# Performance work log

Hardware: AMD Instinct MI355X
Metric: run time of the kernel (lower is better)

The kernel has to match this reference:

```python
import jax, jax.numpy as jnp
import numpy as np

B, T, C = 2, 2048, 1024
NUM_HEADS = 16
HEAD_DIM = C // NUM_HEADS
TEMP = 1.0
LN_EPS = 1e-6


def setup_inputs() -> dict:
    key = jax.random.key(0)
    kx, kqw, kpw = jax.random.split(key, 3)
    x = jax.random.normal(kx, (B, T, C), dtype=jnp.float32)
    # causal mask, broadcastable to [B, H, T, T]
    mask = jnp.tril(jnp.ones((T, T), dtype=bool))[None, None, :, :]
    # LayerNorm params (flax defaults: scale=1, bias=0)
    ln_scale = jnp.ones((C,), dtype=jnp.float32)
    ln_bias = jnp.zeros((C,), dtype=jnp.float32)
    # xavier_uniform init for dense kernels, zero bias (torch_linear)
    lim_qkv = float(np.sqrt(6.0 / (C + 3 * C)))
    qkv_w = jax.random.uniform(kqw, (C, 3 * C), jnp.float32, -lim_qkv, lim_qkv)
    qkv_b = jnp.zeros((3 * C,), dtype=jnp.float32)
    lim_p = float(np.sqrt(6.0 / (C + C)))
    proj_w = jax.random.uniform(kpw, (C, C), jnp.float32, -lim_p, lim_p)
    proj_b = jnp.zeros((C,), dtype=jnp.float32)
    return {"x": x, "mask": mask, "ln_scale": ln_scale, "ln_bias": ln_bias,
            "qkv_w": qkv_w, "qkv_b": qkv_b, "proj_w": proj_w, "proj_b": proj_b}


def reference(x, mask, ln_scale, ln_bias, qkv_w, qkv_b, proj_w, proj_b):
    b, t, c = x.shape
    # LayerNorm (eps=1e-6, flax default)
    mu = jnp.mean(x, axis=-1, keepdims=True)
    var = jnp.mean(jnp.square(x - mu), axis=-1, keepdims=True)
    xn = (x - mu) * jax.lax.rsqrt(var + LN_EPS) * ln_scale + ln_bias
    # fused QKV projection
    qkv = xn @ qkv_w + qkv_b
    q, k, v = jnp.split(qkv, 3, axis=-1)
    q = q.reshape(b, t, NUM_HEADS, HEAD_DIM) / TEMP
    k = k.reshape(b, t, NUM_HEADS, HEAD_DIM)
    v = v.reshape(b, t, NUM_HEADS, HEAD_DIM)
    # scaled dot-product attention with mask (eval path: no dropout)
    q = q / jnp.sqrt(jnp.float32(HEAD_DIM)).astype(x.dtype)
    scores = jnp.einsum('bqhd,bkhd->bhqk', q, k)  # [B,H,T,T]
    big_neg = jnp.finfo(x.dtype).min
    scores = jnp.where(mask, scores, big_neg)
    attn_weights = jax.nn.softmax(scores, axis=-1).astype(x.dtype)
    out = jnp.einsum('bhqk,bkhd->bqhd', attn_weights, v).reshape(b, t, c)
    return out @ proj_w + proj_b
```

## Files before the change

kernel.cpp:

```cpp
#include <hip/hip_runtime.h>
#include <cstdint>
#include <math.h>

#define DEV __device__ __forceinline__

typedef unsigned int u32;
typedef unsigned short u16;
typedef __attribute__((ext_vector_type(4))) float f32x4;
typedef __attribute__((ext_vector_type(4))) u32 u32x4;
typedef __attribute__((ext_vector_type(2))) u32 u32x2;
typedef __attribute__((ext_vector_type(8))) __bf16 bf16x8;

static_assert(sizeof(bf16x8) == 16, "bf16x8 must be 16B");

static constexpr int Tn = 2048, Cn = 1024;
static constexpr int Mrows = 2 * Tn;
static constexpr float QSCALE2 = 0.125f * 1.44269504088896f;

DEV u16 f2bf_rne(float f) {
  u32 u = __builtin_bit_cast(u32, f);
  u32 r = u + 0x7fffu + ((u >> 16) & 1u);
  return (u16)(r >> 16);
}
DEV float bf2f(u16 h) {
  u32 u = ((u32)h) << 16;
  return __builtin_bit_cast(float, u);
}
DEV u32 pack2bf(float a, float b) {
  return (u32)f2bf_rne(a) | ((u32)f2bf_rne(b) << 16);
}
DEV float fexp2(float x) {
#if __has_builtin(__builtin_amdgcn_exp2f)
  return __builtin_amdgcn_exp2f(x);
#else
  return exp2f(x);
#endif
}

DEV void stage16(const void* g, void* l) {
#if __has_builtin(__builtin_amdgcn_global_load_lds)
  __builtin_amdgcn_global_load_lds(
      (__attribute__((address_space(1))) u32*)(uintptr_t)g,
      (__attribute__((address_space(3))) u32*)l, 16, 0, 0);
#else
  *(u32x4*)l = *(const u32x4*)g;
#endif
}

__global__ __launch_bounds__(256) void ln_kernel(const float* __restrict__ x,
                                                 const float* __restrict__ sc,
                                                 const float* __restrict__ bi,
                                                 u16* __restrict__ xn) {
  int row = blockIdx.x;
  int t = threadIdx.x;
  const float* xr = x + (size_t)row * Cn;
  f32x4 v = *(const f32x4*)(xr + t * 4);
  float s = v.x + v.y + v.z + v.w;
  float s2 = v.x * v.x + v.y * v.y + v.z * v.z + v.w * v.w;
#pragma unroll
  for (int off = 1; off < 64; off <<= 1) {
    s += __shfl_xor(s, off);
    s2 += __shfl_xor(s2, off);
  }
  __shared__ float red[8];
  if ((t & 63) == 0) {
    red[(t >> 6) * 2] = s;
    red[(t >> 6) * 2 + 1] = s2;
  }
  __syncthreads();
  s = red[0] + red[2] + red[4] + red[6];
  s2 = red[1] + red[3] + red[5] + red[7];
  float mean = s * (1.0f / Cn);
  float var = s2 * (1.0f / Cn) - mean * mean;
  float rstd = rsqrtf(var + 1e-6f);
  f32x4 g = *(const f32x4*)(sc + t * 4);
  f32x4 b = *(const f32x4*)(bi + t * 4);
  u32 lo = pack2bf((v.x - mean) * rstd * g.x + b.x, (v.y - mean) * rstd * g.y + b.y);
  u32 hi = pack2bf((v.z - mean) * rstd * g.z + b.z, (v.w - mean) * rstd * g.w + b.w);
  u32x2 pack = {lo, hi};
  *(u32x2*)(xn + (size_t)row * Cn + t * 4) = pack;
}

__global__ __launch_bounds__(256) void transpose_cast2(const float* __restrict__ qkv_w,
                                                       u16* __restrict__ wqkv,
                                                       const float* __restrict__ proj_w,
                                                       u16* __restrict__ wproj) {
  __shared__ float tile[32][33];
  int bx = blockIdx.x;
  const float* src;
  u16* dst;
  int Cc;
  if (bx < 96) {
    src = qkv_w; dst = wqkv; Cc = 3072;
  } else {
    src = proj_w; dst = wproj; Cc = 1024; bx -= 96;
  }
  int tx = threadIdx.x, ty = threadIdx.y;
  int c0 = bx * 32, r0 = blockIdx.y * 32;
#pragma unroll
  for (int k = 0; k < 4; ++k)
    tile[ty + 8 * k][tx] = src[(size_t)(r0 + ty + 8 * k) * Cc + c0 + tx];
  __syncthreads();
#pragma unroll
  for (int k = 0; k < 4; ++k)
    dst[(size_t)(c0 + ty + 8 * k) * 1024 + r0 + tx] = f2bf_rne(tile[tx][ty + 8 * k]);
}

__global__ __launch_bounds__(256) void vt_prep(const u16* __restrict__ qkvm,
                                               u16* __restrict__ vt) {
  __shared__ u16 tile[32][33];
  int bh = blockIdx.z;
  int b = bh >> 4, h = bh & 15;
  int t0 = blockIdx.x * 32, d0 = blockIdx.y * 32;
  int tx = threadIdx.x, ty = threadIdx.y;
#pragma unroll
  for (int k = 0; k < 4; ++k)
    tile[ty + 8 * k][tx] =
        qkvm[(size_t)(b * Tn + t0 + ty + 8 * k) * 3072 + 2 * Cn + h * 64 + d0 + tx];
  __syncthreads();
#pragma unroll
  for (int k = 0; k < 4; ++k)
    vt[((size_t)bh * 64 + d0 + ty + 8 * k) * 2048 + t0 + tx] = tile[tx][ty + 8 * k];
}

template <bool OUT_F32, bool QKV_SCALE>
__global__ __launch_bounds__(256, 3) void gemm_kernel(const u16* __restrict__ A,
                                                      const u16* __restrict__ Bt,
                                                      const float* __restrict__ bias,
                                                      void* __restrict__ Cout,
                                                      int Nsz, int Ksz) {
  __shared__ u16 As[128 * 32];
  __shared__ u16 Bs[128 * 32];
  int t = threadIdx.x;
  int l = t & 63, w = t >> 6;
  int quad = l >> 4, c16 = l & 15;
  int wm = w & 1, wn = w >> 1;
  int m0 = blockIdx.y * 128, n0 = blockIdx.x * 128;

  f32x4 acc[4][4];
#pragma unroll
  for (int mt = 0; mt < 4; ++mt)
#pragma unroll
    for (int nt = 0; nt < 4; ++nt) acc[mt][nt] = (f32x4){0.f, 0.f, 0.f, 0.f};

  for (int kk = 0; kk < Ksz; kk += 32) {
#pragma unroll
    for (int i = 0; i < 2; ++i) {
      int c = t + i * 256;
      int m = c >> 2, k8 = (c & 3) ^ ((m >> 1) & 3);
      stage16(A + (size_t)(m0 + m) * Ksz + kk + k8 * 8, (char*)As + c * 16);
    }
#pragma unroll
    for (int i = 0; i < 2; ++i) {
      int c = t + i * 256;
      int n = c >> 2, k8 = (c & 3) ^ ((n >> 1) & 3);
      stage16(Bt + (size_t)(n0 + n) * Ksz + kk + k8 * 8, (char*)Bs + c * 16);
    }
    __syncthreads();
    bf16x8 af[4], bf[4];
#pragma unroll
    for (int mt = 0; mt < 4; ++mt) {
      int m = wm * 64 + mt * 16 + c16;
      int LC = m * 4 + (quad ^ ((m >> 1) & 3));
      af[mt] = *(const bf16x8*)((const char*)As + LC * 16);
    }
#pragma unroll
    for (int nt = 0; nt < 4; ++nt) {
      int n = wn * 64 + nt * 16 + c16;
      int LC = n * 4 + (quad ^ ((n >> 1) & 3));
      bf[nt] = *(const bf16x8*)((const char*)Bs + LC * 16);
    }
#pragma unroll
    for (int mt = 0; mt < 4; ++mt)
#pragma unroll
      for (int nt = 0; nt < 4; ++nt)
        acc[mt][nt] = __builtin_amdgcn_mfma_f32_16x16x32_bf16(af[mt], bf[nt],
                                                              acc[mt][nt], 0, 0, 0);
    __syncthreads();
  }
#pragma unroll
  for (int mt = 0; mt < 4; ++mt) {
    int row = m0 + wm * 64 + mt * 16 + quad * 4;
#pragma unroll
    for (int nt = 0; nt < 4; ++nt) {
      int col = n0 + wn * 64 + nt * 16 + c16;
      float bv = bias[col];
      float scale = (QKV_SCALE && col < 1024) ? QSCALE2 : 1.0f;
#pragma unroll
      for (int r = 0; r < 4; ++r) {
        float v = (acc[mt][nt][r] + bv) * scale;
        if (OUT_F32)
          ((float*)Cout)[(size_t)(row + r) * Nsz + col] = v;
        else
          ((u16*)Cout)[(size_t)(row + r) * Nsz + col] = f2bf_rne(v);
      }
    }
  }
}

__constant__ int4 chunk_tab[24] = {
    {15, 0, 8, 0}, {15, 8, 8, 1}, {14, 0, 8, 0}, {7, 0, 8, -1},
    {14, 8, 7, 1}, {13, 0, 7, 0}, {13, 7, 7, 1}, {12, 0, 7, 0}, {6, 0, 7, -1},
    {12, 7, 6, 1}, {11, 0, 6, 0}, {11, 6, 6, 1}, {10, 0, 6, 0}, {5, 0, 6, -1},
    {10, 6, 5, 1}, {9, 0, 5, 0}, {9, 5, 5, 1}, {8, 0, 5, 0}, {4, 0, 5, -1},
    {8, 5, 4, 1}, {3, 0, 4, -1},
    {2, 0, 3, -1},
    {1, 0, 2, -1},
    {0, 0, 1, -1}};

__global__ __launch_bounds__(256, 2) void flash_kernel(const u16* __restrict__ qkv,
                                                       const u16* __restrict__ vt,
                                                       u16* __restrict__ aout,
                                                       u16* __restrict__ Op,
                                                       float* __restrict__ ml) {
  int4 ck = chunk_tab[blockIdx.x >> 5];
  int bh = blockIdx.x & 31;
  int qt = ck.x, k0 = ck.y, kend = ck.y + ck.z, half = ck.w;
  int b = bh >> 4, h = bh & 15;
  int t = threadIdx.x, l = t & 63, w = t >> 6;
  int quad = l >> 4, c16 = l & 15;
  int q0 = qt * 128;
  const u16* __restrict__ vtb = vt + (size_t)bh * 64 * 2048;

  __shared__ u16 Ks[128 * 64];
  __shared__ u16 Ps[128 * 128];

  bf16x8 qf[2][2];
#pragma unroll
  for (int nt = 0; nt < 2; ++nt)
#pragma unroll
    for (int ks = 0; ks < 2; ++ks)
      qf[nt][ks] = *(const bf16x8*)(qkv +
          (size_t)(b * Tn + q0 + w * 32 + nt * 16 + c16) * 3072 +
          h * 64 + ks * 32 + quad * 8);

  float mrow[2] = {-1e30f, -1e30f};
  float lrow[2] = {0.f, 0.f};
  f32x4 o[2][4];
#pragma unroll
  for (int mq = 0; mq < 2; ++mq)
#pragma unroll
    for (int dt = 0; dt < 4; ++dt) o[mq][dt] = (f32x4){0.f, 0.f, 0.f, 0.f};

  for (int kt = k0; kt < kend; ++kt) {
#pragma unroll
    for (int i = 0; i < 4; ++i) {
      int c = t + i * 256;
      int key = c >> 3, d8 = (c & 7) ^ (key & 7);
      stage16(qkv + (size_t)(b * Tn + kt * 128 + key) * 3072 + Cn + h * 64 + d8 * 8,
              (char*)Ks + c * 16);
    }
    bf16x8 vfc[4], vfn[4];
#pragma unroll
    for (int dt = 0; dt < 4; ++dt)
      vfc[dt] = *(const bf16x8*)(vtb + (size_t)(dt * 16 + c16) * 2048 + kt * 128 +
                                 quad * 8);
    __syncthreads();

    f32x4 s[8][2];
#pragma unroll
    for (int mt = 0; mt < 8; ++mt)
#pragma unroll
      for (int nt = 0; nt < 2; ++nt) s[mt][nt] = (f32x4){0.f, 0.f, 0.f, 0.f};
#pragma unroll
    for (int mt = 0; mt < 8; ++mt) {
#pragma unroll
      for (int ks = 0; ks < 2; ++ks) {
        int key = mt * 16 + c16;
        int d8 = ks * 4 + quad;
        int LC = key * 8 + (d8 ^ (key & 7));
        bf16x8 kf = *(const bf16x8*)((const char*)Ks + LC * 16);
#pragma unroll
        for (int nt = 0; nt < 2; ++nt)
          s[mt][nt] = __builtin_amdgcn_mfma_f32_16x16x32_bf16(kf, qf[nt][ks],
                                                              s[mt][nt], 0, 0, 0);
      }
    }
    if (kt == qt) {
#pragma unroll
      for (int mt = 0; mt < 8; ++mt)
#pragma unroll
        for (int nt = 0; nt < 2; ++nt)
#pragma unroll
          for (int r = 0; r < 4; ++r) {
            int key = kt * 128 + mt * 16 + quad * 4 + r;
            int q = q0 + w * 32 + nt * 16 + c16;
            if (key > q) s[mt][nt][r] = -1e30f;
          }
    }
    float alph[2];
#pragma unroll
    for (int nt = 0; nt < 2; ++nt) {
      float rm = -1e30f;
#pragma unroll
      for (int mt = 0; mt < 8; ++mt)
#pragma unroll
        for (int r = 0; r < 4; ++r) rm = fmaxf(rm, s[mt][nt][r]);
      rm = fmaxf(rm, __shfl_xor(rm, 16));
      rm = fmaxf(rm, __shfl_xor(rm, 32));
      float mnew = fmaxf(mrow[nt], rm);
      alph[nt] = fexp2(mrow[nt] - mnew);
      mrow[nt] = mnew;
      float rs = 0.f;
#pragma unroll
      for (int mt = 0; mt < 8; ++mt)
#pragma unroll
        for (int r = 0; r < 4; ++r) {
          float e = fexp2(s[mt][nt][r] - mnew);
          s[mt][nt][r] = e;
          rs += e;
        }
      rs += __shfl_xor(rs, 16);
      rs += __shfl_xor(rs, 32);
      lrow[nt] = lrow[nt] * alph[nt] + rs;
    }
#pragma unroll
    for (int mq = 0; mq < 2; ++mq)
#pragma unroll
      for (int r = 0; r < 4; ++r) {
        float a = __shfl(alph[mq], quad * 4 + r);
#pragma unroll
        for (int dt = 0; dt < 4; ++dt) o[mq][dt][r] *= a;
      }
#pragma unroll
    for (int mt = 0; mt < 8; ++mt)
#pragma unroll
      for (int nt = 0; nt < 2; ++nt) {
        int q = w * 32 + nt * 16 + c16;
        int kc = mt * 4 + quad;
        int LC = q * 32 + (kc ^ ((q & 15) << 1));
        u32x2 pk = {pack2bf(s[mt][nt][0], s[mt][nt][1]),
                    pack2bf(s[mt][nt][2], s[mt][nt][3])};
        *(u32x2*)((char*)Ps + LC * 8) = pk;
      }
#pragma unroll
    for (int ks = 0; ks < 4; ++ks) {
      if (ks < 3) {
#pragma unroll
        for (int dt = 0; dt < 4; ++dt)
          vfn[dt] = *(const bf16x8*)(vtb + (size_t)(dt * 16 + c16) * 2048 +
                                     kt * 128 + (ks + 1) * 32 + quad * 8);
      }
      bf16x8 pa[2];
#pragma unroll
      for (int mq = 0; mq < 2; ++mq) {
        int q = w * 32 + mq * 16 + c16;
        int kc = ks * 8 + quad * 2;
        int LC = q * 32 + (kc ^ ((q & 15) << 1));
        pa[mq] = *(const bf16x8*)((const char*)Ps + LC * 8);
      }
#pragma unroll
      for (int dt = 0; dt < 4; ++dt)
#pragma unroll
        for (int mq = 0; mq < 2; ++mq)
          o[mq][dt] = __builtin_amdgcn_mfma_f32_16x16x32_bf16(pa[mq], vfc[dt],
                                                              o[mq][dt], 0, 0, 0);
#pragma unroll
      for (int dt = 0; dt < 4; ++dt) vfc[dt] = vfn[dt];
    }
    __syncthreads();
  }

  float linv[2] = {1.0f / lrow[0], 1.0f / lrow[1]};
  if (half < 0) {
#pragma unroll
    for (int mq = 0; mq < 2; ++mq)
#pragma unroll
      for (int r = 0; r < 4; ++r) {
        float li = __shfl(linv[mq], quad * 4 + r);
        int q = q0 + w * 32 + mq * 16 + quad * 4 + r;
#pragma unroll
        for (int dt = 0; dt < 4; ++dt)
          aout[(size_t)(b * Tn + q) * 1024 + h * 64 + dt * 16 + c16] =
              f2bf_rne(o[mq][dt][r] * li);
      }
  } else {
    int ps = ((qt - 8) * 32 + bh) * 2 + half;
#pragma unroll
    for (int mq = 0; mq < 2; ++mq)
#pragma unroll
      for (int r = 0; r < 4; ++r) {
        float li = __shfl(linv[mq], quad * 4 + r);
        int qr = w * 32 + mq * 16 + quad * 4 + r;
#pragma unroll
        for (int dt = 0; dt < 4; ++dt)
          Op[((size_t)ps * 128 + qr) * 64 + dt * 16 + c16] =
              f2bf_rne(o[mq][dt][r] * li);
      }
    if (quad == 0) {
#pragma unroll
      for (int nt = 0; nt < 2; ++nt) {
        int qr = w * 32 + nt * 16 + c16;
        ml[((size_t)ps * 128 + qr) * 2] = mrow[nt];
        ml[((size_t)ps * 128 + qr) * 2 + 1] = lrow[nt];
      }
    }
  }
}

__global__ __launch_bounds__(256) void combine_kernel(const u16* __restrict__ Op,
                                                      const float* __restrict__ ml,
                                                      u16* __restrict__ aout) {
  int qt = 8 + (blockIdx.x >> 5);
  int bh = blockIdx.x & 31;
  int b = bh >> 4, h = bh & 15;
  int ps0 = ((qt - 8) * 32 + bh) * 2;
  int d = threadIdx.x & 63, rq = threadIdx.x >> 6;
  for (int r = 0; r < 32; ++r) {
    int row = rq * 32 + r;
    float m0 = ml[((size_t)ps0 * 128 + row) * 2];
    float l0 = ml[((size_t)ps0 * 128 + row) * 2 + 1];
    float m1 = ml[((size_t)(ps0 + 1) * 128 + row) * 2];
    float l1 = ml[((size_t)(ps0 + 1) * 128 + row) * 2 + 1];
    float M = fmaxf(m0, m1);
    float w0 = fexp2(m0 - M) * l0, w1 = fexp2(m1 - M) * l1;
    float inv = 1.0f / (w0 + w1);
    float o0 = bf2f(Op[((size_t)ps0 * 128 + row) * 64 + d]);
    float o1 = bf2f(Op[((size_t)(ps0 + 1) * 128 + row) * 64 + d]);
    aout[(size_t)(b * Tn + qt * 128 + row) * 1024 + h * 64 + d] =
        f2bf_rne((w0 * o0 + w1 * o1) * inv);
  }
}

extern "C" void kernel_launch(void* const* d_in, const int* in_sizes, int n_in,
                              void* d_out, int out_size, void* d_ws, size_t ws_size,
                              hipStream_t stream) {
  const float* x = (const float*)d_in[0];
  const float* ln_s = (const float*)d_in[2];
  const float* ln_b = (const float*)d_in[3];
  const float* qkv_w = (const float*)d_in[4];
  const float* qkv_b = (const float*)d_in[5];
  const float* proj_w = (const float*)d_in[6];
  const float* proj_b = (const float*)d_in[7];
  float* out = (float*)d_out;
  char* ws = (char*)d_ws;

  u16* xn = (u16*)ws;
  u16* wqkv = (u16*)(ws + (8ull << 20));
  u16* wproj = (u16*)(ws + (14ull << 20));
  u16* qkvm = (u16*)(ws + (16ull << 20));
  u16* attn = (u16*)(ws + (40ull << 20));
  u16* vt = (u16*)(ws + (48ull << 20));
  u16* Op = (u16*)ws;
  float* ml = (float*)(ws + (8ull << 20));

  ln_kernel<<<Mrows, 256, 0, stream>>>(x, ln_s, ln_b, xn);
  transpose_cast2<<<dim3(128, 32), dim3(32, 8), 0, stream>>>(qkv_w, wqkv, proj_w,
                                                             wproj);
  gemm_kernel<false, true><<<dim3(24, 32), 256, 0, stream>>>(xn, wqkv, qkv_b, qkvm,
                                                             3072, 1024);
  vt_prep<<<dim3(64, 2, 32), dim3(32, 8), 0, stream>>>(qkvm, vt);
  flash_kernel<<<768, 256, 0, stream>>>(qkvm, vt, attn, Op, ml);
  combine_kernel<<<256, 256, 0, stream>>>(Op, ml, attn);
  gemm_kernel<true, false><<<dim3(8, 32), 256, 0, stream>>>(attn, wproj, proj_b, out,
                                                            1024, 1024);
}
```

Before: 234.6 us.

## Merge prep kernels, fuse V-transpose into QKV GEMM, load K directly from global

Combines the LayerNorm and weight transpose-cast kernels into one launch, and removes the separate vt_prep kernel by having the QKV GEMM epilogue write V already transposed. In the flash kernel, K tiles are no longer staged in LDS. Each wave loads K fragments straight from global memory with a double-buffered register prefetch, which drops the per-iteration LDS staging and one barrier. This trades fewer launches and less LDS traffic for redundant, less coalesced global K reads across waves and strided 8-byte V stores in the GEMM epilogue.

```diff
diff --git a/kernel.cpp b/kernel.cpp
--- a/kernel.cpp
+++ b/kernel.cpp
@@ -14,7 +14,6 @@
 static_assert(sizeof(bf16x8) == 16, "bf16x8 must be 16B");
 
 static constexpr int Tn = 2048, Cn = 1024;
-static constexpr int Mrows = 2 * Tn;
 static constexpr float QSCALE2 = 0.125f * 1.44269504088896f;
 
 DEV u16 f2bf_rne(float f) {
@@ -47,87 +46,73 @@
 #endif
 }
 
-__global__ __launch_bounds__(256) void ln_kernel(const float* __restrict__ x,
-                                                 const float* __restrict__ sc,
-                                                 const float* __restrict__ bi,
-                                                 u16* __restrict__ xn) {
-  int row = blockIdx.x;
+__global__ __launch_bounds__(256) void pre_kernel(const float* __restrict__ x,
+                                                  const float* __restrict__ sc,
+                                                  const float* __restrict__ bi,
+                                                  u16* __restrict__ xn,
+                                                  const float* __restrict__ qkv_w,
+                                                  u16* __restrict__ wqkv,
+                                                  const float* __restrict__ proj_w,
+                                                  u16* __restrict__ wproj) {
+  __shared__ float shm[32 * 33];
   int t = threadIdx.x;
-  const float* xr = x + (size_t)row * Cn;
-  f32x4 v = *(const f32x4*)(xr + t * 4);
-  float s = v.x + v.y + v.z + v.w;
-  float s2 = v.x * v.x + v.y * v.y + v.z * v.z + v.w * v.w;
-#pragma unroll
-  for (int off = 1; off < 64; off <<= 1) {
-    s += __shfl_xor(s, off);
-    s2 += __shfl_xor(s2, off);
-  }
-  __shared__ float red[8];
-  if ((t & 63) == 0) {
-    red[(t >> 6) * 2] = s;
-    red[(t >> 6) * 2 + 1] = s2;
-  }
-  __syncthreads();
-  s = red[0] + red[2] + red[4] + red[6];
-  s2 = red[1] + red[3] + red[5] + red[7];
-  float mean = s * (1.0f / Cn);
-  float var = s2 * (1.0f / Cn) - mean * mean;
-  float rstd = rsqrtf(var + 1e-6f);
-  f32x4 g = *(const f32x4*)(sc + t * 4);
-  f32x4 b = *(const f32x4*)(bi + t * 4);
-  u32 lo = pack2bf((v.x - mean) * rstd * g.x + b.x, (v.y - mean) * rstd * g.y + b.y);
-  u32 hi = pack2bf((v.z - mean) * rstd * g.z + b.z, (v.w - mean) * rstd * g.w + b.w);
-  u32x2 pack = {lo, hi};
-  *(u32x2*)(xn + (size_t)row * Cn + t * 4) = pack;
-}
-
-__global__ __launch_bounds__(256) void transpose_cast2(const float* __restrict__ qkv_w,
-                                                       u16* __restrict__ wqkv,
-                                                       const float* __restrict__ proj_w,
-                                                       u16* __restrict__ wproj) {
-  __shared__ float tile[32][33];
-  int bx = blockIdx.x;
-  const float* src;
-  u16* dst;
-  int Cc;
-  if (bx < 96) {
-    src = qkv_w; dst = wqkv; Cc = 3072;
+  if (blockIdx.x < 4096) {
+    int row = blockIdx.x;
+    const float* xr = x + (size_t)row * Cn;
+    f32x4 v = *(const f32x4*)(xr + t * 4);
+    float s = v.x + v.y + v.z + v.w;
+    float s2 = v.x * v.x + v.y * v.y + v.z * v.z + v.w * v.w;
+#pragma unroll
+    for (int off = 1; off < 64; off <<= 1) {
+      s += __shfl_xor(s, off);
+      s2 += __shfl_xor(s2, off);
+    }
+    if ((t & 63) == 0) {
+      shm[(t >> 6) * 2] = s;
+      shm[(t >> 6) * 2 + 1] = s2;
+    }
+    __syncthreads();
+    s = shm[0] + shm[2] + shm[4] + shm[6];
+    s2 = shm[1] + shm[3] + shm[5] + shm[7];
+    float mean = s * (1.0f / Cn);
+    float var = s2 * (1.0f / Cn) - mean * mean;
+    float rstd = rsqrtf(var + 1e-6f);
+    f32x4 g = *(const f32x4*)(sc + t * 4);
+    f32x4 b = *(const f32x4*)(bi + t * 4);
+    u32 lo = pack2bf((v.x - mean) * rstd * g.x + b.x, (v.y - mean) * rstd * g.y + b.y);
+    u32 hi = pack2bf((v.z - mean) * rstd * g.z + b.z, (v.w - mean) * rstd * g.w + b.w);
+    u32x2 pack = {lo, hi};
+    *(u32x2*)(xn + (size_t)row * Cn + t * 4) = pack;
   } else {
-    src = proj_w; dst = wproj; Cc = 1024; bx -= 96;
-  }
-  int tx = threadIdx.x, ty = threadIdx.y;
-  int c0 = bx * 32, r0 = blockIdx.y * 32;
-#pragma unroll
-  for (int k = 0; k < 4; ++k)
-    tile[ty + 8 * k][tx] = src[(size_t)(r0 + ty + 8 * k) * Cc + c0 + tx];
-  __syncthreads();
-#pragma unroll
-  for (int k = 0; k < 4; ++k)
-    dst[(size_t)(c0 + ty + 8 * k) * 1024 + r0 + tx] = f2bf_rne(tile[tx][ty + 8 * k]);
-}
-
-__global__ __launch_bounds__(256) void vt_prep(const u16* __restrict__ qkvm,
-                                               u16* __restrict__ vt) {
-  __shared__ u16 tile[32][33];
-  int bh = blockIdx.z;
-  int b = bh >> 4, h = bh & 15;
-  int t0 = blockIdx.x * 32, d0 = blockIdx.y * 32;
-  int tx = threadIdx.x, ty = threadIdx.y;
-#pragma unroll
-  for (int k = 0; k < 4; ++k)
-    tile[ty + 8 * k][tx] =
-        qkvm[(size_t)(b * Tn + t0 + ty + 8 * k) * 3072 + 2 * Cn + h * 64 + d0 + tx];
-  __syncthreads();
-#pragma unroll
-  for (int k = 0; k < 4; ++k)
-    vt[((size_t)bh * 64 + d0 + ty + 8 * k) * 2048 + t0 + tx] = tile[tx][ty + 8 * k];
-}
-
-template <bool OUT_F32, bool QKV_SCALE>
+    int idx = blockIdx.x - 4096;
+    int bx = idx & 127, by = idx >> 7;
+    const float* src;
+    u16* dst;
+    int Cc;
+    if (bx < 96) {
+      src = qkv_w; dst = wqkv; Cc = 3072;
+    } else {
+      src = proj_w; dst = wproj; Cc = 1024; bx -= 96;
+    }
+    int tx = t & 31, ty = t >> 5;
+    int c0 = bx * 32, r0 = by * 32;
+#pragma unroll
+    for (int k = 0; k < 4; ++k)
+      shm[(ty + 8 * k) * 33 + tx] = src[(size_t)(r0 + ty + 8 * k) * Cc + c0 + tx];
+    __syncthreads();
+#pragma unroll
+    for (int k = 0; k < 4; ++k)
+      dst[(size_t)(c0 + ty + 8 * k) * 1024 + r0 + tx] =
+          f2bf_rne(shm[tx * 33 + ty + 8 * k]);
+  }
+}
+
+template <bool OUT_F32, bool QKV>
 __global__ __launch_bounds__(256, 3) void gemm_kernel(const u16* __restrict__ A,
                                                       const u16* __restrict__ Bt,
                                                       const float* __restrict__ bias,
                                                       void* __restrict__ Cout,
+                                                      u16* __restrict__ vtp,
                                                       int Nsz, int Ksz) {
   __shared__ u16 As[128 * 32];
   __shared__ u16 Bs[128 * 32];
@@ -185,14 +170,22 @@
     for (int nt = 0; nt < 4; ++nt) {
       int col = n0 + wn * 64 + nt * 16 + c16;
       float bv = bias[col];
-      float scale = (QKV_SCALE && col < 1024) ? QSCALE2 : 1.0f;
-#pragma unroll
-      for (int r = 0; r < 4; ++r) {
-        float v = (acc[mt][nt][r] + bv) * scale;
-        if (OUT_F32)
-          ((float*)Cout)[(size_t)(row + r) * Nsz + col] = v;
-        else
-          ((u16*)Cout)[(size_t)(row + r) * Nsz + col] = f2bf_rne(v);
+      if (QKV && col >= 2048) {
+        int hd = col - 2048;
+        int bb = row >> 11, tt = row & 2047;
+        u32x2 pk = {pack2bf(acc[mt][nt][0] + bv, acc[mt][nt][1] + bv),
+                    pack2bf(acc[mt][nt][2] + bv, acc[mt][nt][3] + bv)};
+        *(u32x2*)(vtp + ((size_t)bb * 1024 + hd) * 2048 + tt) = pk;
+      } else {
+        float scale = (QKV && col < 1024) ? QSCALE2 : 1.0f;
+#pragma unroll
+        for (int r = 0; r < 4; ++r) {
+          float v = (acc[mt][nt][r] + bv) * scale;
+          if (OUT_F32)
+            ((float*)Cout)[(size_t)(row + r) * Nsz + col] = v;
+          else
+            ((u16*)Cout)[(size_t)(row + r) * Nsz + col] = f2bf_rne(v);
+        }
       }
     }
   }
@@ -221,8 +214,9 @@
   int quad = l >> 4, c16 = l & 15;
   int q0 = qt * 128;
   const u16* __restrict__ vtb = vt + (size_t)bh * 64 * 2048;
-
-  __shared__ u16 Ks[128 * 64];
+  const u16* __restrict__ kb =
+      qkv + ((size_t)(b * Tn) + c16) * 3072 + Cn + h * 64 + quad * 8;
+
   __shared__ u16 Ps[128 * 128];
 
   bf16x8 qf[2][2];
@@ -243,19 +237,18 @@
     for (int dt = 0; dt < 4; ++dt) o[mq][dt] = (f32x4){0.f, 0.f, 0.f, 0.f};
 
   for (int kt = k0; kt < kend; ++kt) {
-#pragma unroll
-    for (int i = 0; i < 4; ++i) {
-      int c = t + i * 256;
-      int key = c >> 3, d8 = (c & 7) ^ (key & 7);
-      stage16(qkv + (size_t)(b * Tn + kt * 128 + key) * 3072 + Cn + h * 64 + d8 * 8,
-              (char*)Ks + c * 16);
-    }
-    bf16x8 vfc[4], vfn[4];
+    bf16x8 vfc[4];
 #pragma unroll
     for (int dt = 0; dt < 4; ++dt)
       vfc[dt] = *(const bf16x8*)(vtb + (size_t)(dt * 16 + c16) * 2048 + kt * 128 +
                                  quad * 8);
-    __syncthreads();
+    const u16* kr = kb + (size_t)kt * 128 * 3072;
+    bf16x8 ka[2][2];
+#pragma unroll
+    for (int p = 0; p < 2; ++p)
+#pragma unroll
+      for (int ks = 0; ks < 2; ++ks)
+        ka[p][ks] = *(const bf16x8*)(kr + (size_t)p * 16 * 3072 + ks * 32);
 
     f32x4 s[8][2];
 #pragma unroll
@@ -265,15 +258,16 @@
 #pragma unroll
     for (int mt = 0; mt < 8; ++mt) {
 #pragma unroll
-      for (int ks = 0; ks < 2; ++ks) {
-        int key = mt * 16 + c16;
-        int d8 = ks * 4 + quad;
-        int LC = key * 8 + (d8 ^ (key & 7));
-        bf16x8 kf = *(const bf16x8*)((const char*)Ks + LC * 16);
+      for (int ks = 0; ks < 2; ++ks)
 #pragma unroll
         for (int nt = 0; nt < 2; ++nt)
-          s[mt][nt] = __builtin_amdgcn_mfma_f32_16x16x32_bf16(kf, qf[nt][ks],
-                                                              s[mt][nt], 0, 0, 0);
+          s[mt][nt] = __builtin_amdgcn_mfma_f32_16x16x32_bf16(
+              ka[mt & 1][ks], qf[nt][ks], s[mt][nt], 0, 0, 0);
+      if (mt < 6) {
+#pragma unroll
+        for (int ks = 0; ks < 2; ++ks)
+          ka[mt & 1][ks] =
+              *(const bf16x8*)(kr + (size_t)(mt + 2) * 16 * 3072 + ks * 32);
       }
     }
     if (kt == qt) {
@@ -335,6 +329,7 @@
       }
 #pragma unroll
     for (int ks = 0; ks < 4; ++ks) {
+      bf16x8 vfn[4];
       if (ks < 3) {
 #pragma unroll
         for (int dt = 0; dt < 4; ++dt)
@@ -355,10 +350,11 @@
         for (int mq = 0; mq < 2; ++mq)
           o[mq][dt] = __builtin_amdgcn_mfma_f32_16x16x32_bf16(pa[mq], vfc[dt],
                                                               o[mq][dt], 0, 0, 0);
-#pragma unroll
-      for (int dt = 0; dt < 4; ++dt) vfc[dt] = vfn[dt];
-    }
-    __syncthreads();
+      if (ks < 3) {
+#pragma unroll
+        for (int dt = 0; dt < 4; ++dt) vfc[dt] = vfn[dt];
+      }
+    }
   }
 
   float linv[2] = {1.0f / lrow[0], 1.0f / lrow[1]};
@@ -444,14 +440,12 @@
   u16* Op = (u16*)ws;
   float* ml = (float*)(ws + (8ull << 20));
 
-  ln_kernel<<<Mrows, 256, 0, stream>>>(x, ln_s, ln_b, xn);
-  transpose_cast2<<<dim3(128, 32), dim3(32, 8), 0, stream>>>(qkv_w, wqkv, proj_w,
-                                                             wproj);
+  pre_kernel<<<8192, 256, 0, stream>>>(x, ln_s, ln_b, xn, qkv_w, wqkv, proj_w,
+                                       wproj);
   gemm_kernel<false, true><<<dim3(24, 32), 256, 0, stream>>>(xn, wqkv, qkv_b, qkvm,
-                                                             3072, 1024);
-  vt_prep<<<dim3(64, 2, 32), dim3(32, 8), 0, stream>>>(qkvm, vt);
+                                                             vt, 3072, 1024);
   flash_kernel<<<768, 256, 0, stream>>>(qkvm, vt, attn, Op, ml);
   combine_kernel<<<256, 256, 0, stream>>>(Op, ml, attn);
   gemm_kernel<true, false><<<dim3(8, 32), 256, 0, stream>>>(attn, wproj, proj_b, out,
-                                                            1024, 1024);
-}
+                                                            nullptr, 1024, 1024);
+}
```

New measurement: 244.4 us. +4.2%, slower.
